# Kernel optimization log

Hardware: AMD Instinct MI355X
Metric: run time of the kernel (lower is better)

Reference implementation:

```python
import jax, jax.numpy as jnp
import numpy as np

B, N, D = 8, 1024, 512
H, HD = 8, 64          # heads, head_dim
E_EDGES = 4096         # num edges (!= N -> mean-pool branch)
NE, NSH, TOPK = 8, 2, 2  # routed experts, shared experts, top-k
DH = 2 * D             # expert hidden dim
EPS = 1e-5
HALT_BONUS = 0.1
AUX_ALPHA = 0.01


def _ln(x, g, b):
    mu = jnp.mean(x, -1, keepdims=True)
    var = jnp.mean(jnp.square(x - mu), -1, keepdims=True)
    return (x - mu) * jax.lax.rsqrt(var + EPS) * g + b


def setup_inputs() -> dict:
    key = jax.random.key(0)
    ks = jax.random.split(key, 20)
    w = lambda k, shp: jax.random.normal(k, shp, jnp.float32) * 0.02
    return {
        'h': jax.random.normal(ks[0], (B, N, D), jnp.float32),
        'edge_features': jax.random.normal(ks[1], (B, E_EDGES, D), jnp.float32),
        'log_A': jnp.zeros((D,), jnp.float32),
        'B_w': w(ks[2], (D, D)), 'B_b': jnp.zeros((D,), jnp.float32),
        'Wq': w(ks[3], (D, D)), 'bq': jnp.zeros((D,), jnp.float32),
        'Wk': w(ks[4], (D, D)), 'bk': jnp.zeros((D,), jnp.float32),
        'Wv': w(ks[5], (D, D)), 'bv': jnp.zeros((D,), jnp.float32),
        'Wo': w(ks[6], (D, D)), 'bo': jnp.zeros((D,), jnp.float32),
        'n1_g': jnp.ones((D,), jnp.float32), 'n1_b': jnp.zeros((D,), jnp.float32),
        'n2_g': jnp.ones((D,), jnp.float32), 'n2_b': jnp.zeros((D,), jnp.float32),
        'n3_g': jnp.ones((D,), jnp.float32), 'n3_b': jnp.zeros((D,), jnp.float32),
        'gate_w': w(ks[7], (D, NE)), 'gate_b': jnp.zeros((NE,), jnp.float32),
        'eW1': w(ks[8], (NE, D, DH)), 'eb1': jnp.zeros((NE, DH), jnp.float32),
        'eW2': w(ks[9], (NE, DH, D)), 'eb2': jnp.zeros((NE, D), jnp.float32),
        'sW1': w(ks[10], (NSH, D, DH)), 'sb1': jnp.zeros((NSH, DH), jnp.float32),
        'sW2': w(ks[11], (NSH, DH, D)), 'sb2': jnp.zeros((NSH, D), jnp.float32),
        'hW1': w(ks[12], (D, D // 2)), 'hb1': jnp.zeros((D // 2,), jnp.float32),
        'hW2': w(ks[13], (D // 2, 1)), 'hb2': jnp.zeros((1,), jnp.float32),
    }


def reference(h, edge_features, log_A, B_w, B_b, Wq, bq, Wk, bk, Wv, bv, Wo, bo,
              n1_g, n1_b, n2_g, n2_b, n3_g, n3_b, gate_w, gate_b,
              eW1, eb1, eW2, eb2, sW1, sb1, sW2, sb2, hW1, hb1, hW2, hb2):
    # --- LTI: h_decay + mean-pooled edge injection (num_edges != num_nodes) ---
    A = -jnp.exp(log_A)                                   # spectral constraint
    edge_inj = edge_features @ B_w + B_b                  # [B,E,D]
    edge_inj = jnp.mean(edge_inj, axis=1, keepdims=True)  # [B,1,D] broadcast
    h_lti = _ln(A * h + edge_inj, n1_g, n1_b)

    # --- attention (faithful to source: no head/node transpose -> [B,N,H,H] scores) ---
    q = (h_lti @ Wq + bq).reshape(B, N, H, HD)
    k = (h_lti @ Wk + bk).reshape(B, N, H, HD)
    v = (h_lti @ Wv + bv).reshape(B, N, H, HD)
    scores = jnp.einsum('bnhd,bngd->bnhg', q, k) / jnp.sqrt(jnp.float32(HD))
    attn = jax.nn.softmax(scores, axis=-1)                # dropout = identity (eval)
    h_attn = jnp.einsum('bnhg,bngd->bnhd', attn, v).reshape(B, N, D) @ Wo + bo
    h2 = _ln(h_lti + h_attn, n2_g, n2_b)

    # --- SparseMoE: top-k routed + shared experts, load-balance aux loss ---
    x = h2.reshape(-1, D)                                 # [T,D]
    T = x.shape[0]
    probs = jax.nn.softmax(x @ gate_w + gate_b, axis=-1)  # [T,NE]
    topv, topi = jax.lax.top_k(probs, TOPK)
    topv = topv / jnp.sum(topv, -1, keepdims=True)        # renormalize top-k
    w_full = jnp.sum(jax.nn.one_hot(topi, NE, dtype=x.dtype) * topv[..., None], axis=1)  # [T,NE]
    hid = jax.nn.silu(jnp.einsum('td,edh->teh', x, eW1) + eb1)   # [T,NE,DH]
    eout = jnp.einsum('teh,ehd->ted', hid, eW2) + eb2            # [T,NE,D]
    routed = jnp.einsum('te,ted->td', w_full, eout)
    shid = jax.nn.silu(jnp.einsum('td,sdh->tsh', x, sW1) + sb1)
    shared = jnp.sum(jnp.einsum('tsh,shd->tsd', shid, sW2) + sb2, axis=1)
    h_moe = (routed + shared).reshape(B, N, D)
    frac = jnp.mean(jnp.sum(jax.nn.one_hot(topi, NE, dtype=x.dtype), axis=1), axis=0)  # tokens per expert
    pmean = jnp.mean(probs, axis=0)
    moe_loss = AUX_ALPHA * NE * jnp.sum(frac * pmean)

    h3 = _ln(h2 + h_moe, n3_g, n3_b)                      # dropout = identity (eval)

    # --- stability loss (source uses .item() -> detached constant) ---
    stab = jax.lax.stop_gradient(jnp.maximum(jnp.max(jnp.exp(log_A)) - 0.95, 0.0))

    # --- ACT halting (cumsum_halt=None path) ---
    halt_logits = (jnp.tanh(h3 @ hW1 + hb1) @ hW2 + hb2)[..., 0]  # [B,N]
    halt_prob = jax.nn.sigmoid(halt_logits)
    cumsum_halt = halt_prob                                # zeros + prob * active(=1)
    return h3, cumsum_halt, halt_prob, stab + moe_loss
```

## Files before the change

### kernel.cpp

```cpp
#include <hip/hip_runtime.h>
#include <hip/hip_bf16.h>

#define TT 8192
#define DD 512

typedef unsigned short u16;
typedef __attribute__((ext_vector_type(8))) short short8;
typedef __attribute__((ext_vector_type(4))) float f32x4;

__device__ __forceinline__ u16 f2b(float f) {
  union { float f; unsigned int i; } w; w.f = f;
  unsigned int x = w.i;
  unsigned int r = (x + 0x7FFFu + ((x >> 16) & 1u)) >> 16;
  if ((x & 0x7F800000u) == 0x7F800000u) r = x >> 16;
  return (u16)r;
}
__device__ __forceinline__ float b2f(u16 u) {
  union { unsigned int i; float f; } w; w.i = ((unsigned int)u) << 16; return w.f;
}

__device__ __forceinline__ void blockReduce2(float& a, float& b, float* s4a, float* s4b) {
  #pragma unroll
  for (int off = 32; off; off >>= 1) { a += __shfl_xor(a, off); b += __shfl_xor(b, off); }
  int wid = threadIdx.x >> 6;
  if ((threadIdx.x & 63) == 0) { s4a[wid] = a; s4b[wid] = b; }
  __syncthreads();
  a = s4a[0] + s4a[1] + s4a[2] + s4a[3];
  b = s4b[0] + s4b[1] + s4b[2] + s4b[3];
}

__global__ __launch_bounds__(256) void k_zero(float* __restrict__ esum) {
  esum[blockIdx.x * 256 + threadIdx.x] = 0.f;
}

__global__ __launch_bounds__(256) void k_zero4(float4* __restrict__ p) {
  p[(size_t)blockIdx.x * 256 + threadIdx.x] = make_float4(0.f, 0.f, 0.f, 0.f);
}

__global__ __launch_bounds__(256) void k_esum(const float* __restrict__ ef, float* __restrict__ esum) {
  int b = blockIdx.x, ec = blockIdx.y, tid = threadIdx.x;
  float a0 = 0.f, a1 = 0.f;
  const float* base = ef + ((size_t)b * 4096 + (size_t)ec * 128) * 512;
  for (int e = 0; e < 128; ++e) {
    a0 += base[(size_t)e * 512 + tid];
    a1 += base[(size_t)e * 512 + tid + 256];
  }
  atomicAdd(&esum[b * 512 + tid], a0);
  atomicAdd(&esum[b * 512 + tid + 256], a1);
}

__global__ __launch_bounds__(256) void k_einj(const float* __restrict__ esum,
                                              const float* __restrict__ Bw, const float* __restrict__ Bb,
                                              float* __restrict__ einj) {
  int idx = blockIdx.x * 256 + threadIdx.x;
  int b = idx >> 9, dp = idx & 511;
  float a = Bb[dp];
  const float inv = 1.f / 4096.f;
  for (int d = 0; d < 512; ++d)
    a = fmaf(esum[b * 512 + d] * inv, Bw[d * 512 + dp], a);
  einj[idx] = a;
}

__global__ __launch_bounds__(256) void k_wsplit(const float* __restrict__ Wq, const float* __restrict__ Wk,
                                                const float* __restrict__ Wv, const float* __restrict__ Wo,
                                                u16* __restrict__ outh, u16* __restrict__ outl) {
  __shared__ float st[64][65];
  int z = blockIdx.z;
  const float* W = z == 0 ? Wq : (z == 1 ? Wk : (z == 2 ? Wv : Wo));
  int k0 = blockIdx.x << 6, n0 = blockIdx.y << 6;
  int tid = threadIdx.x;
  int r = tid >> 2, c4 = (tid & 3) << 4;
  #pragma unroll
  for (int j = 0; j < 16; j += 4) {
    float4 v = *(const float4*)(W + (size_t)(k0 + r) * 512 + n0 + c4 + j);
    st[c4 + j + 0][r] = v.x; st[c4 + j + 1][r] = v.y;
    st[c4 + j + 2][r] = v.z; st[c4 + j + 3][r] = v.w;
  }
  __syncthreads();
  int n = tid >> 2, kb = (tid & 3) << 4;
  u16 h8[8] __attribute__((aligned(16)));
  u16 l8[8] __attribute__((aligned(16)));
  size_t obase = (size_t)z * 262144 + (size_t)(n0 + n) * 512 + k0 + kb;
  #pragma unroll
  for (int half = 0; half < 2; ++half) {
    #pragma unroll
    for (int j = 0; j < 8; ++j) {
      float val = st[n][kb + half * 8 + j];
      h8[j] = f2b(val);
      l8[j] = f2b(val - b2f(h8[j]));
    }
    *(uint4*)(outh + obase + half * 8) = *(uint4*)h8;
    *(uint4*)(outl + obase + half * 8) = *(uint4*)l8;
  }
}

__global__ __launch_bounds__(256) void k_wt(const float* __restrict__ W, u16* __restrict__ Wt,
                                            int K, int N) {
  __shared__ float st[64][65];
  int z = blockIdx.z;
  W += (size_t)z * K * N; Wt += (size_t)z * K * N;
  int k0 = blockIdx.x << 6, n0 = blockIdx.y << 6;
  int tid = threadIdx.x;
  int r = tid >> 2, c4 = (tid & 3) << 4;
  #pragma unroll
  for (int j = 0; j < 16; j += 4) {
    float4 v = *(const float4*)(W + (size_t)(k0 + r) * N + n0 + c4 + j);
    st[c4 + j + 0][r] = v.x; st[c4 + j + 1][r] = v.y;
    st[c4 + j + 2][r] = v.z; st[c4 + j + 3][r] = v.w;
  }
  __syncthreads();
  int n = tid >> 2, kb = (tid & 3) << 4;
  u16 h8[8] __attribute__((aligned(16)));
  size_t obase = (size_t)(n0 + n) * K + k0 + kb;
  #pragma unroll
  for (int half = 0; half < 2; ++half) {
    #pragma unroll
    for (int j = 0; j < 8; ++j) h8[j] = f2b(st[n][kb + half * 8 + j]);
    *(uint4*)(Wt + obase + half * 8) = *(uint4*)h8;
  }
}

__global__ __launch_bounds__(256) void k_lti(const float* __restrict__ h, const float* __restrict__ lA,
                                             const float* __restrict__ einj,
                                             const float* __restrict__ g, const float* __restrict__ be,
                                             u16* __restrict__ Xh, u16* __restrict__ Xl, int seg0) {
  __shared__ float sa[4], sb[4];
  int rowg = seg0 + blockIdx.x, b = rowg >> 10, tid = threadIdx.x;
  int d0 = tid, d1 = tid + 256;
  size_t gbase = (size_t)rowg * 512;
  size_t lbase = (size_t)blockIdx.x * 512;
  float v0 = -expf(lA[d0]) * h[gbase + d0] + einj[b * 512 + d0];
  float v1 = -expf(lA[d1]) * h[gbase + d1] + einj[b * 512 + d1];
  float s = v0 + v1, ss = v0 * v0 + v1 * v1;
  blockReduce2(s, ss, sa, sb);
  float mu = s * (1.f / 512.f);
  float var = fmaxf(ss * (1.f / 512.f) - mu * mu, 0.f);
  float r = rsqrtf(var + 1e-5f);
  float o0 = (v0 - mu) * r * g[d0] + be[d0];
  float o1 = (v1 - mu) * r * g[d1] + be[d1];
  u16 h0 = f2b(o0), h1 = f2b(o1);
  Xh[lbase + d0] = h0; Xl[lbase + d0] = f2b(o0 - b2f(h0));
  Xh[lbase + d1] = h1; Xl[lbase + d1] = f2b(o1 - b2f(h1));
}

__global__ __launch_bounds__(256) void k_ln_res2(const u16* __restrict__ Xh, const u16* __restrict__ Xl,
                                                 const float* __restrict__ Bv,
                                                 const float* __restrict__ g, const float* __restrict__ be,
                                                 float* __restrict__ outf, u16* __restrict__ outb) {
  __shared__ float sa[4], sb[4];
  int tid = threadIdx.x, d0 = tid, d1 = tid + 256;
  size_t base = (size_t)blockIdx.x * 512;
  float v0 = b2f(Xh[base + d0]) + b2f(Xl[base + d0]) + Bv[base + d0];
  float v1 = b2f(Xh[base + d1]) + b2f(Xl[base + d1]) + Bv[base + d1];
  float s = v0 + v1, ss = v0 * v0 + v1 * v1;
  blockReduce2(s, ss, sa, sb);
  float mu = s * (1.f / 512.f);
  float var = fmaxf(ss * (1.f / 512.f) - mu * mu, 0.f);
  float r = rsqrtf(var + 1e-5f);
  float o0 = (v0 - mu) * r * g[d0] + be[d0];
  float o1 = (v1 - mu) * r * g[d1] + be[d1];
  outf[base + d0] = o0;
  outf[base + d1] = o1;
  if (outb) { outb[base + d0] = f2b(o0); outb[base + d1] = f2b(o1); }
}

__global__ __launch_bounds__(256) void k_ln_res(const float* __restrict__ A, const float* __restrict__ Bv,
                                                const float* __restrict__ g, const float* __restrict__ be,
                                                float* __restrict__ outf, u16* __restrict__ outb) {
  __shared__ float sa[4], sb[4];
  int tid = threadIdx.x, d0 = tid, d1 = tid + 256;
  size_t base = (size_t)blockIdx.x * 512;
  float v0 = A[base + d0] + Bv[base + d0];
  float v1 = A[base + d1] + Bv[base + d1];
  float s = v0 + v1, ss = v0 * v0 + v1 * v1;
  blockReduce2(s, ss, sa, sb);
  float mu = s * (1.f / 512.f);
  float var = fmaxf(ss * (1.f / 512.f) - mu * mu, 0.f);
  float r = rsqrtf(var + 1e-5f);
  float o0 = (v0 - mu) * r * g[d0] + be[d0];
  float o1 = (v1 - mu) * r * g[d1] + be[d1];
  outf[base + d0] = o0;
  outf[base + d1] = o1;
  if (outb) { outb[base + d0] = f2b(o0); outb[base + d1] = f2b(o1); }
}

template<int NOUT>
__global__ __launch_bounds__(512, 4) void gemm_sp3(
    const u16* __restrict__ Xh, const u16* __restrict__ Xl, int lda,
    const u16* __restrict__ Wth, const u16* __restrict__ Wtl,
    const float* __restrict__ b0c, const float* __restrict__ b1c, const float* __restrict__ b2c,
    float* __restrict__ C0, float* __restrict__ C1, float* __restrict__ C2) {
  const float* bias = b0c; float* C = C0;
  const u16* Wh = Wth; const u16* Wl = Wtl;
  if (NOUT == 3) {
    int z = blockIdx.z;
    Wh += (size_t)z * 262144; Wl += (size_t)z * 262144;
    if (z == 1) { bias = b1c; C = C1; }
    else if (z == 2) { bias = b2c; C = C2; }
  }
  const int bm = blockIdx.y << 7, bn = blockIdx.x << 7;
  __shared__ u16 Ah[2][128][40];
  __shared__ u16 Al[2][128][40];
  __shared__ u16 Bh[2][128][40];
  __shared__ u16 Bl[2][128][40];
  const int tid = threadIdx.x;
  const int sr = tid >> 2, sk = (tid & 3) << 3;
  const int wv = tid >> 6, lane = tid & 63, q = lane >> 4, m16 = lane & 15;
  const int wr = (wv >> 2) << 6;
  const int wc = (wv & 3) << 5;
  const u16* ahr = Xh + (size_t)(bm + sr) * lda;
  const u16* alr = Xl + (size_t)(bm + sr) * lda;
  const u16* bhr = Wh + (size_t)(bn + sr) * 512;
  const u16* blr = Wl + (size_t)(bn + sr) * 512;
  f32x4 acc[4][2];
  #pragma unroll
  for (int m = 0; m < 4; ++m)
    #pragma unroll
    for (int n = 0; n < 2; ++n)
      #pragma unroll
      for (int i = 0; i < 4; ++i) acc[m][n][i] = 0.f;

  uint4 rah = *(const uint4*)(ahr + sk);
  uint4 ral = *(const uint4*)(alr + sk);
  uint4 rbh = *(const uint4*)(bhr + sk);
  uint4 rbl = *(const uint4*)(blr + sk);
  *(uint4*)&Ah[0][sr][sk] = rah;
  *(uint4*)&Al[0][sr][sk] = ral;
  *(uint4*)&Bh[0][sr][sk] = rbh;
  *(uint4*)&Bl[0][sr][sk] = rbl;
  __syncthreads();
  int cur = 0;
  for (int k0 = 0; k0 < 512; k0 += 32) {
    if (k0 + 32 < 512) {
      rah = *(const uint4*)(ahr + k0 + 32 + sk);
      ral = *(const uint4*)(alr + k0 + 32 + sk);
      rbh = *(const uint4*)(bhr + k0 + 32 + sk);
      rbl = *(const uint4*)(blr + k0 + 32 + sk);
    }
    short8 ahf[4], alf[4];
    #pragma unroll
    for (int m = 0; m < 4; ++m) {
      ahf[m] = *(const short8*)&Ah[cur][wr + m * 16 + m16][q * 8];
      alf[m] = *(const short8*)&Al[cur][wr + m * 16 + m16][q * 8];
    }
    #pragma unroll
    for (int n = 0; n < 2; ++n) {
      short8 bhf = *(const short8*)&Bh[cur][wc + n * 16 + m16][q * 8];
      short8 blf = *(const short8*)&Bl[cur][wc + n * 16 + m16][q * 8];
      #pragma unroll
      for (int m = 0; m < 4; ++m) {
        acc[m][n] = __builtin_amdgcn_mfma_f32_16x16x32_bf16(ahf[m], bhf, acc[m][n], 0, 0, 0);
        acc[m][n] = __builtin_amdgcn_mfma_f32_16x16x32_bf16(alf[m], bhf, acc[m][n], 0, 0, 0);
        acc[m][n] = __builtin_amdgcn_mfma_f32_16x16x32_bf16(ahf[m], blf, acc[m][n], 0, 0, 0);
      }
    }
    if (k0 + 32 < 512) {
      *(uint4*)&Ah[cur ^ 1][sr][sk] = rah;
      *(uint4*)&Al[cur ^ 1][sr][sk] = ral;
      *(uint4*)&Bh[cur ^ 1][sr][sk] = rbh;
      *(uint4*)&Bl[cur ^ 1][sr][sk] = rbl;
      __syncthreads();
      cur ^= 1;
    }
  }
  #pragma unroll
  for (int n = 0; n < 2; ++n) {
    int col = bn + wc + n * 16 + m16;
    float bb = bias[col];
    #pragma unroll
    for (int m = 0; m < 4; ++m) {
      #pragma unroll
      for (int i = 0; i < 4; ++i) {
        int rl = bm + wr + m * 16 + q * 4 + i;
        C[(size_t)rl * 512 + col] = acc[m][n][i] + bb;
      }
    }
  }
}

__global__ __launch_bounds__(64) void k_attn(const float* __restrict__ q, const float* __restrict__ k,
                                             const float* __restrict__ v,
                                             u16* __restrict__ aohl) {
  __shared__ float qs[512], ks[512], vs[512], at[64];
  size_t t = blockIdx.x;
  int lane = threadIdx.x;
  for (int i = lane; i < 512; i += 64) {
    qs[i] = q[t * 512 + i]; ks[i] = k[t * 512 + i]; vs[i] = v[t * 512 + i];
  }
  __syncthreads();
  int h = lane >> 3, g = lane & 7;
  float s = 0.f;
  #pragma unroll 8
  for (int d = 0; d < 64; ++d) s = fmaf(qs[h * 64 + d], ks[g * 64 + d], s);
  s *= 0.125f;
  float m = s;
  #pragma unroll
  for (int off = 1; off < 8; off <<= 1) m = fmaxf(m, __shfl_xor(m, off));
  float ex = expf(s - m);
  float sum = ex;
  #pragma unroll
  for (int off = 1; off < 8; off <<= 1) sum += __shfl_xor(sum, off);
  at[lane] = ex / sum;
  __syncthreads();
  #pragma unroll
  for (int j = 0; j < 8; ++j) {
    int d = lane + j * 64, hh = d >> 6, hd = d & 63;
    float acc = 0.f;
    #pragma unroll
    for (int gg = 0; gg < 8; ++gg) acc = fmaf(at[hh * 8 + gg], vs[gg * 64 + hd], acc);
    u16 hi = f2b(acc);
    aohl[t * 1024 + d] = hi;
    aohl[t * 1024 + 512 + d] = f2b(acc - b2f(hi));
  }
}

__global__ __launch_bounds__(256) void k_gateA(const float* __restrict__ h2, const float* __restrict__ gw,
                                               const float* __restrict__ gb, float* __restrict__ probs,
                                               int* __restrict__ sel, float2* __restrict__ wpair) {
  int lane = threadIdx.x & 63, wid = threadIdx.x >> 6;
  int t = blockIdx.x * 4 + wid;
  const float* x = h2 + (size_t)t * 512;
  float acc[8] = {};
  for (int d = lane; d < 512; d += 64) {
    float xv = x[d];
    float4 g0 = *(const float4*)(gw + d * 8);
    float4 g1 = *(const float4*)(gw + d * 8 + 4);
    acc[0] = fmaf(xv, g0.x, acc[0]); acc[1] = fmaf(xv, g0.y, acc[1]);
    acc[2] = fmaf(xv, g0.z, acc[2]); acc[3] = fmaf(xv, g0.w, acc[3]);
    acc[4] = fmaf(xv, g1.x, acc[4]); acc[5] = fmaf(xv, g1.y, acc[5]);
    acc[6] = fmaf(xv, g1.z, acc[6]); acc[7] = fmaf(xv, g1.w, acc[7]);
  }
  #pragma unroll
  for (int off = 32; off; off >>= 1)
    #pragma unroll
    for (int e = 0; e < 8; ++e) acc[e] += __shfl_xor(acc[e], off);
  if (lane == 0) {
    float m = -1e30f;
    #pragma unroll
    for (int e = 0; e < 8; ++e) { acc[e] += gb[e]; m = fmaxf(m, acc[e]); }
    float p[8], sum = 0.f;
    #pragma unroll
    for (int e = 0; e < 8; ++e) { p[e] = expf(acc[e] - m); sum += p[e]; }
    float inv = 1.f / sum;
    #pragma unroll
    for (int e = 0; e < 8; ++e) { p[e] *= inv; probs[t * 8 + e] = p[e]; }
    int i1 = 0; float m1 = p[0];
    #pragma unroll
    for (int e = 1; e < 8; ++e) if (p[e] > m1) { m1 = p[e]; i1 = e; }
    int i2 = -1; float m2 = -1.f;
    #pragma unroll
    for (int e = 0; e < 8; ++e) if (e != i1 && p[e] > m2) { m2 = p[e]; i2 = e; }
    if (i2 < 0) i2 = (i1 + 1) & 7;
    float den = m1 + m2;
    float invs = (den > 0.f) ? 1.f / den : 0.f;
    sel[t] = i1 | (i2 << 4);
    wpair[t] = make_float2(m1 * invs, m2 * invs);
  }
}

__global__ __launch_bounds__(256) void k_gateB(const int* __restrict__ sel, const float2* __restrict__ wpair,
                                               int* __restrict__ toklist, float* __restrict__ wlist,
                                               int* __restrict__ cnt) {
  int e = blockIdx.x;
  int tid = threadIdx.x, lane = tid & 63, wv = tid >> 6;
  __shared__ int wsum[4];
  int base = 0;
  for (int t0 = 0; t0 < 8192; t0 += 256) {
    int t = t0 + tid;
    int s = sel[t];
    int i1 = s & 15, i2 = (s >> 4) & 15;
    bool f = (i1 == e) || (i2 == e);
    float wt = (i1 == e) ? wpair[t].x : ((i2 == e) ? wpair[t].y : 0.f);
    unsigned long long m = __ballot(f);
    int rank = __popcll(m & ((1ull << lane) - 1ull));
    int wtot = __popcll(m);
    if (lane == 0) wsum[wv] = wtot;
    __syncthreads();
    int prev = 0;
    for (int ww = 0; ww < wv; ++ww) prev += wsum[ww];
    int tot = wsum[0] + wsum[1] + wsum[2] + wsum[3];
    if (f) {
      int pos = base + prev + rank;
      toklist[e * 8192 + pos] = t;
      wlist[e * 8192 + pos] = wt;
    }
    base += tot;
    __syncthreads();
  }
  if (tid == 0) cnt[e] = base;
}

template<int XMODE, int ACT, int OUTMODE, int EXPERT>
__global__ __launch_bounds__(256) void mfma_gemm(
    const float* __restrict__ Xf, const u16* __restrict__ Xb,
    const float* __restrict__ Wg, const float* __restrict__ biasg,
    float* __restrict__ C, u16* __restrict__ C16,
    const int* __restrict__ toklist, const float* __restrict__ wlist,
    const int* __restrict__ cnt, int M, int K, int N, int chunk0,
    size_t hidstride, float* __restrict__ moe) {
  int e = EXPERT ? blockIdx.z : 0;
  const float* W = Wg + (size_t)e * K * N;
  const float* bias = biasg + (size_t)e * N;
  int Mloc = M;
  if (EXPERT) {
    int ce = cnt[e]; if (ce > 8192) ce = 8192;
    Mloc = ce - chunk0;
    if (XMODE == 1) Xb += (size_t)e * hidstride;
    if (OUTMODE == 2) C16 += (size_t)e * hidstride;
  }
  const int bm = blockIdx.y << 6, bn = blockIdx.x << 6;
  if (EXPERT && bm >= Mloc) return;
  __shared__ u16 As[64][40];
  __shared__ u16 Bs[64][40];
  __shared__ int rows[64];
  const int tid = threadIdx.x;
  if (EXPERT && XMODE == 2 && tid < 64) {
    int ce = cnt[e]; if (ce > 8192) ce = 8192;
    int r = chunk0 + bm + tid;
    rows[tid] = toklist[e * 8192 + (r < ce ? r : chunk0)] & 8191;
  }
  const int srow = tid >> 2;
  const int skg = (tid & 3) << 3;
  const int wv = tid >> 6, lane = tid & 63, q = lane >> 4, m16 = lane & 15;
  f32x4 acc[4];
  #pragma unroll
  for (int c = 0; c < 4; ++c)
    #pragma unroll
    for (int i = 0; i < 4; ++i) acc[c][i] = 0.f;

  for (int k0 = 0; k0 < K; k0 += 32) {
    __syncthreads();
    {
      u16 a8[8] __attribute__((aligned(16)));
      if (XMODE == 1) {
        *(uint4*)a8 = *(const uint4*)(Xb + (size_t)(bm + srow) * K + k0 + skg);
      } else {
        const float* src = (XMODE == 2) ? (Xf + (size_t)rows[srow] * K + k0 + skg)
                                        : (Xf + (size_t)(bm + srow) * K + k0 + skg);
        float4 x0 = *(const float4*)(src);
        float4 x1 = *(const float4*)(src + 4);
        a8[0] = f2b(x0.x); a8[1] = f2b(x0.y); a8[2] = f2b(x0.z); a8[3] = f2b(x0.w);
        a8[4] = f2b(x1.x); a8[5] = f2b(x1.y); a8[6] = f2b(x1.z); a8[7] = f2b(x1.w);
      }
      *(uint4*)&As[srow][skg] = *(uint4*)a8;
    }
    {
      u16 b8[8] __attribute__((aligned(16)));
      const float* src = W + (size_t)(k0 + skg) * N + bn + srow;
      #pragma unroll
      for (int j = 0; j < 8; ++j) b8[j] = f2b(src[(size_t)j * N]);
      *(uint4*)&Bs[srow][skg] = *(uint4*)b8;
    }
    __syncthreads();
    short8 af = *(const short8*)&As[wv * 16 + m16][q * 8];
    #pragma unroll
    for (int c = 0; c < 4; ++c) {
      short8 bf = *(const short8*)&Bs[c * 16 + m16][q * 8];
      acc[c] = __builtin_amdgcn_mfma_f32_16x16x32_bf16(af, bf, acc[c], 0, 0, 0);
    }
  }
  #pragma unroll
  for (int c = 0; c < 4; ++c) {
    int col = bn + c * 16 + m16;
    float bb = bias[col];
    #pragma unroll
    for (int i = 0; i < 4; ++i) {
      int rl = bm + wv * 16 + q * 4 + i;
      if (EXPERT && rl >= Mloc) continue;
      float v = acc[c][i] + bb;
      if (ACT == 1) v = v / (1.f + expf(-v));
      else if (ACT == 2) v = tanhf(v);
      if (OUTMODE == 0) C[(size_t)rl * N + col] = v;
      else if (OUTMODE == 1) C[(size_t)rl * N + col] += v;
      else if (OUTMODE == 2) C16[(size_t)rl * N + col] = f2b(v);
      else {
        int rg = chunk0 + rl;
        int tok = toklist[e * 8192 + rg] & 8191;
        float wt = wlist[e * 8192 + rg];
        atomicAdd(&moe[(size_t)tok * 512 + col], v * wt);
      }
    }
  }
}

template<int XMODE, int ACT, int OUTMODE, int EXPERT>
__global__ __launch_bounds__(512, 4) void mfma_gemm3(
    const u16* __restrict__ Xb, const u16* __restrict__ Wt, const float* __restrict__ biasg,
    float* __restrict__ C, u16* __restrict__ C16,
    const int* __restrict__ toklist, const float* __restrict__ wlist,
    const int* __restrict__ cnt, int M, int K, int N, int chunk0,
    size_t hidstride, float* __restrict__ moe) {
  int e = EXPERT ? blockIdx.z : 0;
  const u16* W = Wt + (size_t)e * K * N;
  const float* bias = biasg + (size_t)e * N;
  int Mloc = M;
  if (EXPERT == 1) {
    int ce = cnt[e]; if (ce > 8192) ce = 8192;
    Mloc = ce - chunk0;
  }
  if (EXPERT) {
    if (XMODE == 3) Xb += (size_t)e * hidstride;
    if (OUTMODE == 2) C16 += (size_t)e * hidstride;
  }
  const int bm = blockIdx.y << 7, bn = blockIdx.x << 7;
  if (EXPERT == 1 && bm >= Mloc) return;
  __shared__ u16 As[2][128][40];
  __shared__ u16 Bs[2][128][40];
  __shared__ int rows[128];
  const int tid = threadIdx.x;
  if (EXPERT == 1 && XMODE == 2) {
    if (tid < 128) {
      int ce = cnt[e]; if (ce > 8192) ce = 8192;
      int r = chunk0 + bm + tid;
      rows[tid] = toklist[e * 8192 + (r < ce ? r : chunk0)] & 8191;
    }
    __syncthreads();
  }
  const int sr = tid >> 2, sk = (tid & 3) << 3;
  const int wv = tid >> 6, lane = tid & 63, q = lane >> 4, m16 = lane & 15;
  const int wr = (wv >> 2) << 6;
  const int wc = (wv & 3) << 5;
  const u16* arow = (XMODE == 2) ? (Xb + (size_t)rows[sr] * K) : (Xb + (size_t)(bm + sr) * K);
  const u16* brow = W + (size_t)(bn + sr) * K;
  f32x4 acc[4][2];
  #pragma unroll
  for (int m = 0; m < 4; ++m)
    #pragma unroll
    for (int n = 0; n < 2; ++n)
      #pragma unroll
      for (int i = 0; i < 4; ++i) acc[m][n][i] = 0.f;

  uint4 ar = *(const uint4*)(arow + sk);
  uint4 br = *(const uint4*)(brow + sk);
  *(uint4*)&As[0][sr][sk] = ar;
  *(uint4*)&Bs[0][sr][sk] = br;
  __syncthreads();
  int cur = 0;
  for (int k0 = 0; k0 < K; k0 += 32) {
    if (k0 + 32 < K) {
      ar = *(const uint4*)(arow + k0 + 32 + sk);
      br = *(const uint4*)(brow + k0 + 32 + sk);
    }
    short8 af[4];
    #pragma unroll
    for (int m = 0; m < 4; ++m)
      af[m] = *(const short8*)&As[cur][wr + m * 16 + m16][q * 8];
    short8 bf[2];
    #pragma unroll
    for (int n = 0; n < 2; ++n)
      bf[n] = *(const short8*)&Bs[cur][wc + n * 16 + m16][q * 8];
    #pragma unroll
    for (int n = 0; n < 2; ++n)
      #pragma unroll
      for (int m = 0; m < 4; ++m)
        acc[m][n] = __builtin_amdgcn_mfma_f32_16x16x32_bf16(af[m], bf[n], acc[m][n], 0, 0, 0);
    if (k0 + 32 < K) {
      *(uint4*)&As[cur ^ 1][sr][sk] = ar;
      *(uint4*)&Bs[cur ^ 1][sr][sk] = br;
      __syncthreads();
      cur ^= 1;
    }
  }
  #pragma unroll
  for (int n = 0; n < 2; ++n) {
    int col = bn + wc + n * 16 + m16;
    float bb = bias[col];
    #pragma unroll
    for (int m = 0; m < 4; ++m) {
      #pragma unroll
      for (int i = 0; i < 4; ++i) {
        int rl = bm + wr + m * 16 + q * 4 + i;
        if (EXPERT == 1 && rl >= Mloc) continue;
        float v = acc[m][n][i] + bb;
        if (ACT == 1) v = v / (1.f + expf(-v));
        else if (ACT == 2) v = tanhf(v);
        if (OUTMODE == 0) C[(size_t)rl * N + col] = v;
        else if (OUTMODE == 1) C[(size_t)rl * N + col] += v;
        else if (OUTMODE == 2) C16[(size_t)rl * N + col] = f2b(v);
        else if (OUTMODE == 3) {
          int rg = chunk0 + rl;
          int tok = toklist[e * 8192 + rg] & 8191;
          float wt = wlist[e * 8192 + rg];
          atomicAdd(&moe[(size_t)tok * 512 + col], v * wt);
        } else {
          atomicAdd(&C[(size_t)rl * N + col], v);
        }
      }
    }
  }
}

__global__ __launch_bounds__(256) void k_halt(const u16* __restrict__ hh, const float* __restrict__ hW2,
                                              const float* __restrict__ hb2, float* __restrict__ out) {
  int lane = threadIdx.x & 63, wid = threadIdx.x >> 6;
  int t = blockIdx.x * 4 + wid;
  const u16* x = hh + (size_t)t * 256;
  float a = b2f(x[lane]) * hW2[lane] + b2f(x[lane + 64]) * hW2[lane + 64] +
            b2f(x[lane + 128]) * hW2[lane + 128] + b2f(x[lane + 192]) * hW2[lane + 192];
  #pragma unroll
  for (int off = 32; off; off >>= 1) a += __shfl_xor(a, off);
  if (lane == 0) {
    float p = 1.f / (1.f + expf(-(a + hb2[0])));
    out[4194304 + t] = p;
    out[4194304 + 8192 + t] = p;
  }
}

__global__ __launch_bounds__(256) void k_final(const float* __restrict__ probs, const int* __restrict__ cnt,
                                               const float* __restrict__ lA, float* __restrict__ out) {
  __shared__ float sp[4][8];
  __shared__ float sm[4];
  int tid = threadIdx.x, lane = tid & 63, wid = tid >> 6;
  float part[8] = {};
  for (int i = tid; i < 8192; i += 256) {
    const float* p = probs + i * 8;
    #pragma unroll
    for (int e = 0; e < 8; ++e) part[e] += p[e];
  }
  #pragma unroll
  for (int off = 32; off; off >>= 1)
    #pragma unroll
    for (int e = 0; e < 8; ++e) part[e] += __shfl_xor(part[e], off);
  float mx = 0.f;
  for (int d = tid; d < 512; d += 256) mx = fmaxf(mx, expf(lA[d]));
  #pragma unroll
  for (int off = 32; off; off >>= 1) mx = fmaxf(mx, __shfl_xor(mx, off));
  if (lane == 0) {
    #pragma unroll
    for (int e = 0; e < 8; ++e) sp[wid][e] = part[e];
    sm[wid] = mx;
  }
  __syncthreads();
  if (tid == 0) {
    float loss = 0.f;
    for (int e = 0; e < 8; ++e) {
      float pm = (sp[0][e] + sp[1][e] + sp[2][e] + sp[3][e]) * (1.f / 8192.f);
      int c = cnt[e]; if (c > 8192) c = 8192;
      loss += (float)c * (1.f / 8192.f) * pm;
    }
    loss *= 0.01f * 8.f;
    float mall = fmaxf(fmaxf(sm[0], sm[1]), fmaxf(sm[2], sm[3]));
    out[4194304 + 16384] = fmaxf(mall - 0.95f, 0.f) + loss;
  }
}

extern "C" void kernel_launch(void* const* d_in, const int* in_sizes, int n_in,
                              void* d_out, int out_size, void* d_ws, size_t ws_size,
                              hipStream_t stream) {
  const float* h   = (const float*)d_in[0];
  const float* ef  = (const float*)d_in[1];
  const float* lA  = (const float*)d_in[2];
  const float* Bw  = (const float*)d_in[3];
  const float* Bb  = (const float*)d_in[4];
  const float* Wq  = (const float*)d_in[5];  const float* bq  = (const float*)d_in[6];
  const float* Wk  = (const float*)d_in[7];  const float* bk  = (const float*)d_in[8];
  const float* Wv  = (const float*)d_in[9];  const float* bv  = (const float*)d_in[10];
  const float* Wo  = (const float*)d_in[11]; const float* bo  = (const float*)d_in[12];
  const float* n1g = (const float*)d_in[13]; const float* n1b = (const float*)d_in[14];
  const float* n2g = (const float*)d_in[15]; const float* n2b = (const float*)d_in[16];
  const float* n3g = (const float*)d_in[17]; const float* n3b = (const float*)d_in[18];
  const float* gw  = (const float*)d_in[19]; const float* gb  = (const float*)d_in[20];
  const float* eW1 = (const float*)d_in[21]; const float* eb1 = (const float*)d_in[22];
  const float* eW2 = (const float*)d_in[23]; const float* eb2 = (const float*)d_in[24];
  const float* sW1 = (const float*)d_in[25]; const float* sb1 = (const float*)d_in[26];
  const float* sW2 = (const float*)d_in[27]; const float* sb2 = (const float*)d_in[28];
  const float* hW1 = (const float*)d_in[29]; const float* hb1 = (const float*)d_in[30];
  const float* hW2 = (const float*)d_in[31]; const float* hb2 = (const float*)d_in[32];
  float* out = (float*)d_out;
  float* ws = (float*)d_ws;

  const size_t R = (size_t)TT * DD;
  const size_t SM = 155648 + 73744;
  size_t wsf = ws_size / 4;
  int S; size_t ARENA;
  bool FAST;
  if (wsf >= 6 * R + SM)      { S = 8192; ARENA = 4 * R; FAST = true; }
  else if (wsf >= 3 * R + SM) { S = 2048; ARENA = R; FAST = false; }
  else                        { S = 512;  ARENA = 1048576; FAST = false; }
  const int CAPE = (int)(ARENA / 4096);
  const int NCH  = 8192 / CAPE;
  const size_t HIDSTRIDE = (size_t)CAPE * 1024;
  const int CAPS = (ARENA / 512 >= 8192) ? 8192 : (int)(ARENA / 512);

  float* f_h2  = ws;
  float* f_moe = ws + R;
  float* arena = ws + 2 * R;
  const size_t SD = (size_t)S * 512;
  u16* f_xh = (u16*)arena;
  u16* f_xl = f_xh + SD;
  float* f_q = arena + SD;
  float* f_k = arena + 2 * SD;
  float* f_v = arena + 3 * SD;
  u16* f_aohl = (u16*)f_q;
  float* f_hp = f_k;
  u16* f_wh = (u16*)f_moe;
  u16* f_wl = f_wh + 4 * 262144;
  u16* f_hid = (u16*)arena;
  u16* f_hh  = (u16*)arena;
  u16* a16 = (u16*)arena;
  const int CAPE_F = 2048, NCH_F = 4;
  const size_t HSF = (size_t)CAPE_F * 1024;
  u16* f_hidF = a16;
  u16* f_eW1t = a16 + 16777216;
  u16* f_eW2t = a16 + 20971520;
  u16* f_h2b  = a16 + 25165824;
  u16* f_sW1t = a16 + 29360128;
  u16* f_sW2t = a16 + 30408704;
  u16* f_h3b  = a16;
  u16* f_hW1t = a16 + 4194304;
  u16* f_hh3  = a16 + 4325376;
  float* smr = ws + 2 * R + ARENA;
  float* f_esum = smr;
  float* f_einj = smr + 4096;
  float* f_probs = smr + 8192;
  float2* f_wpair = (float2*)(smr + 8192 + 65536);
  float* f_wlist = smr + 8192 + 65536 + 16384;
  int* ip = (int*)(smr + 8192 + 65536 + 16384 + 65536);
  int* sel = ip; int* cnt = ip + 8192; int* toklist = ip + 8192 + 16;

  k_zero<<<16, 256, 0, stream>>>(f_esum);
  k_esum<<<dim3(8, 32), 256, 0, stream>>>(ef, f_esum);
  k_einj<<<16, 256, 0, stream>>>(f_esum, Bw, Bb, f_einj);
  k_wsplit<<<dim3(8, 8, 4), 256, 0, stream>>>(Wq, Wk, Wv, Wo, f_wh, f_wl);

  for (int s = 0; s < TT / S; ++s) {
    int seg0 = s * S;
    k_lti<<<S, 256, 0, stream>>>(h, lA, f_einj, n1g, n1b, f_xh, f_xl, seg0);
    gemm_sp3<3><<<dim3(4, S / 128, 3), 512, 0, stream>>>(
        f_xh, f_xl, 512, f_wh, f_wl, bq, bk, bv, f_q, f_k, f_v);
    k_attn<<<S, 64, 0, stream>>>(f_q, f_k, f_v, f_aohl);
    gemm_sp3<1><<<dim3(4, S / 128, 1), 512, 0, stream>>>(
        f_aohl, f_aohl + 512, 1024, f_wh + 3 * 262144, f_wl + 3 * 262144,
        bo, nullptr, nullptr, f_hp, nullptr, nullptr);
    k_ln_res2<<<S, 256, 0, stream>>>(f_xh, f_xl, f_hp, n2g, n2b,
                                     f_h2 + (size_t)seg0 * 512,
                                     FAST ? f_h2b + (size_t)seg0 * 512 : nullptr);
  }

  k_gateA<<<TT / 4, 256, 0, stream>>>(f_h2, gw, gb, f_probs, sel, f_wpair);
  k_gateB<<<8, 256, 0, stream>>>(sel, f_wpair, toklist, f_wlist, cnt);

  if (FAST) {
    k_zero4<<<4096, 256, 0, stream>>>((float4*)f_moe);
    k_wt<<<dim3(8, 16, 8), 256, 0, stream>>>(eW1, f_eW1t, 512, 1024);
    k_wt<<<dim3(16, 8, 8), 256, 0, stream>>>(eW2, f_eW2t, 1024, 512);
    k_wt<<<dim3(8, 16, 2), 256, 0, stream>>>(sW1, f_sW1t, 512, 1024);
    k_wt<<<dim3(16, 8, 2), 256, 0, stream>>>(sW2, f_sW2t, 1024, 512);

    mfma_gemm3<1,1,2,2><<<dim3(8, 64, 2), 512, 0, stream>>>(
        f_h2b, f_sW1t, sb1, nullptr, f_hidF, nullptr, nullptr, nullptr,
        TT, 512, 1024, 0, (size_t)TT * 1024, nullptr);
    mfma_gemm3<3,0,4,2><<<dim3(4, 64, 2), 512, 0, stream>>>(
        f_hidF, f_sW2t, sb2, f_moe, nullptr, nullptr, nullptr, nullptr,
        TT, 1024, 512, 0, (size_t)TT * 1024, nullptr);

    for (int c = 0; c < NCH_F; ++c) {
      mfma_gemm3<2,1,2,1><<<dim3(8, CAPE_F / 128, 8), 512, 0, stream>>>(
          f_h2b, f_eW1t, eb1, nullptr, f_hidF, toklist, nullptr, cnt,
          CAPE_F, 512, 1024, c * CAPE_F, HSF, nullptr);
      mfma_gemm3<3,0,3,1><<<dim3(4, CAPE_F / 128, 8), 512, 0, stream>>>(
          f_hidF, f_eW2t, eb2, nullptr, nullptr, toklist, f_wlist, cnt,
          CAPE_F, 1024, 512, c * CAPE_F, HSF, f_moe);
    }

    k_ln_res<<<TT, 256, 0, stream>>>(f_h2, f_moe, n3g, n3b, out, f_h3b);
    k_wt<<<dim3(8, 4, 1), 256, 0, stream>>>(hW1, f_hW1t, 512, 256);
    mfma_gemm3<1,2,2,0><<<dim3(2, 64), 512, 0, stream>>>(
        f_h3b, f_hW1t, hb1, nullptr, f_hh3, nullptr, nullptr, nullptr,
        TT, 512, 256, 0, 0, nullptr);
    k_halt<<<TT / 4, 256, 0, stream>>>(f_hh3, hW2, hb2, out);
  } else {
    for (int sx = 0; sx < 2; ++sx)
      for (int c = 0; c < TT / CAPS; ++c) {
        const float* xs = f_h2 + (size_t)c * CAPS * 512;
        float* ms = f_moe + (size_t)c * CAPS * 512;
        mfma_gemm<0,1,2,0><<<dim3(16, CAPS / 64), 256, 0, stream>>>(
            xs, nullptr, sW1 + (size_t)sx * 524288, sb1 + sx * 1024,
            nullptr, f_hid, nullptr, nullptr, nullptr, CAPS, 512, 1024, 0, 0, nullptr);
        if (sx == 0)
          mfma_gemm<1,0,0,0><<<dim3(8, CAPS / 64), 256, 0, stream>>>(
              nullptr, f_hid, sW2, sb2, ms, nullptr, nullptr, nullptr, nullptr, CAPS, 1024, 512, 0, 0, nullptr);
        else
          mfma_gemm<1,0,1,0><<<dim3(8, CAPS / 64), 256, 0, stream>>>(
              nullptr, f_hid, sW2 + 524288, sb2 + 512, ms, nullptr, nullptr, nullptr, nullptr, CAPS, 1024, 512, 0, 0, nullptr);
      }
    for (int c = 0; c < NCH; ++c) {
      mfma_gemm<2,1,2,1><<<dim3(16, CAPE / 64, 8), 256, 0, stream>>>(
          f_h2, nullptr, eW1, eb1, nullptr, f_hid, toklist, nullptr, cnt,
          CAPE, 512, 1024, c * CAPE, HIDSTRIDE, nullptr);
      mfma_gemm<1,0,3,1><<<dim3(8, CAPE / 64, 8), 256, 0, stream>>>(
          nullptr, f_hid, eW2, eb2, nullptr, nullptr, toklist, f_wlist, cnt,
          CAPE, 1024, 512, c * CAPE, HIDSTRIDE, f_moe);
    }
    k_ln_res<<<TT, 256, 0, stream>>>(f_h2, f_moe, n3g, n3b, out, nullptr);
    mfma_gemm<0,2,2,0><<<dim3(4, 128), 256, 0, stream>>>(
        out, nullptr, hW1, hb1, nullptr, f_hh, nullptr, nullptr, nullptr, TT, 512, 256, 0, 0, nullptr);
    k_halt<<<TT / 4, 256, 0, stream>>>(f_hh, hW2, hb2, out);
  }

  k_final<<<1, 256, 0, stream>>>(f_probs, cnt, lA, out);
}
```

Before: 691.1 us.

## Pack routed experts into one grouped GEMM and fuse gating into LayerNorm

Routed-expert GEMMs now use one launch over a padded, prefix-offset packed layout: each 128-row tile looks up its expert from per-expert offsets. This replaces the four chunked launches per layer, which also spawned empty blocks for lightly loaded experts. The gate softmax and top-2 selection are fused into the second LayerNorm kernel, removing a separate pass over h2. The first shared-expert down-projection writes the output directly and the second adds into it, so the zero-fill kernel is dropped. The cost is a serial prefix-sum kernel and an 8-iteration per-block expert search. The fused gate also adds a cross-wave reduction to every LayerNorm block.

Result: faster. 637.7 us (-7.7%).

```diff
diff --git a/kernel.cpp b/kernel.cpp
--- a/kernel.cpp
+++ b/kernel.cpp
@@ -31,10 +31,6 @@
 
 __global__ __launch_bounds__(256) void k_zero(float* __restrict__ esum) {
   esum[blockIdx.x * 256 + threadIdx.x] = 0.f;
-}
-
-__global__ __launch_bounds__(256) void k_zero4(float4* __restrict__ p) {
-  p[(size_t)blockIdx.x * 256 + threadIdx.x] = make_float4(0.f, 0.f, 0.f, 0.f);
 }
 
 __global__ __launch_bounds__(256) void k_esum(const float* __restrict__ ef, float* __restrict__ esum) {
@@ -146,8 +142,12 @@
 __global__ __launch_bounds__(256) void k_ln_res2(const u16* __restrict__ Xh, const u16* __restrict__ Xl,
                                                  const float* __restrict__ Bv,
                                                  const float* __restrict__ g, const float* __restrict__ be,
-                                                 float* __restrict__ outf, u16* __restrict__ outb) {
+                                                 float* __restrict__ outf, u16* __restrict__ outb,
+                                                 const float* __restrict__ gw, const float* __restrict__ gb,
+                                                 float* __restrict__ probs, int* __restrict__ sel,
+                                                 float2* __restrict__ wpair) {
   __shared__ float sa[4], sb[4];
+  __shared__ float s8[4][8];
   int tid = threadIdx.x, d0 = tid, d1 = tid + 256;
   size_t base = (size_t)blockIdx.x * 512;
   float v0 = b2f(Xh[base + d0]) + b2f(Xl[base + d0]) + Bv[base + d0];
@@ -162,6 +162,53 @@
   outf[base + d0] = o0;
   outf[base + d1] = o1;
   if (outb) { outb[base + d0] = f2b(o0); outb[base + d1] = f2b(o1); }
+  if (probs) {
+    float4 g0a = *(const float4*)(gw + d0 * 8);
+    float4 g0b = *(const float4*)(gw + d0 * 8 + 4);
+    float4 g1a = *(const float4*)(gw + d1 * 8);
+    float4 g1b = *(const float4*)(gw + d1 * 8 + 4);
+    float ga[8] = { o0 * g0a.x + o1 * g1a.x, o0 * g0a.y + o1 * g1a.y,
+                    o0 * g0a.z + o1 * g1a.z, o0 * g0a.w + o1 * g1a.w,
+                    o0 * g0b.x + o1 * g1b.x, o0 * g0b.y + o1 * g1b.y,
+                    o0 * g0b.z + o1 * g1b.z, o0 * g0b.w + o1 * g1b.w };
+    #pragma unroll
+    for (int off = 32; off; off >>= 1)
+      #pragma unroll
+      for (int e = 0; e < 8; ++e) ga[e] += __shfl_xor(ga[e], off);
+    int lane = tid & 63, wid = tid >> 6;
+    if (lane == 0) {
+      #pragma unroll
+      for (int e = 0; e < 8; ++e) s8[wid][e] = ga[e];
+    }
+    __syncthreads();
+    if (tid == 0) {
+      int t = blockIdx.x;
+      float acc[8];
+      float m = -1e30f;
+      #pragma unroll
+      for (int e = 0; e < 8; ++e) {
+        acc[e] = s8[0][e] + s8[1][e] + s8[2][e] + s8[3][e] + gb[e];
+        m = fmaxf(m, acc[e]);
+      }
+      float p[8], sum = 0.f;
+      #pragma unroll
+      for (int e = 0; e < 8; ++e) { p[e] = expf(acc[e] - m); sum += p[e]; }
+      float inv = 1.f / sum;
+      #pragma unroll
+      for (int e = 0; e < 8; ++e) { p[e] *= inv; probs[t * 8 + e] = p[e]; }
+      int i1 = 0; float m1 = p[0];
+      #pragma unroll
+      for (int e = 1; e < 8; ++e) if (p[e] > m1) { m1 = p[e]; i1 = e; }
+      int i2 = -1; float m2 = -1.f;
+      #pragma unroll
+      for (int e = 0; e < 8; ++e) if (e != i1 && p[e] > m2) { m2 = p[e]; i2 = e; }
+      if (i2 < 0) i2 = (i1 + 1) & 7;
+      float den = m1 + m2;
+      float invs = (den > 0.f) ? 1.f / den : 0.f;
+      sel[t] = i1 | (i2 << 4);
+      wpair[t] = make_float2(m1 * invs, m2 * invs);
+    }
+  }
 }
 
 __global__ __launch_bounds__(256) void k_ln_res(const float* __restrict__ A, const float* __restrict__ Bv,
@@ -182,6 +229,17 @@
   outf[base + d0] = o0;
   outf[base + d1] = o1;
   if (outb) { outb[base + d0] = f2b(o0); outb[base + d1] = f2b(o1); }
+}
+
+__global__ __launch_bounds__(64) void k_prefix(const int* __restrict__ cnt, int* __restrict__ off) {
+  if (threadIdx.x == 0) {
+    int acc = 0;
+    for (int e = 0; e < 8; ++e) {
+      off[e] = acc;
+      int c = cnt[e]; if (c > 8192) c = 8192;
+      acc += (c + 127) & ~127;
+    }
+  }
 }
 
 template<int NOUT>
@@ -490,29 +548,46 @@
     const int* __restrict__ toklist, const float* __restrict__ wlist,
     const int* __restrict__ cnt, int M, int K, int N, int chunk0,
     size_t hidstride, float* __restrict__ moe) {
-  int e = EXPERT ? blockIdx.z : 0;
+  const int bm = blockIdx.y << 7, bn = blockIdx.x << 7;
+  int e = 0, offe = 0;
+  int Mloc = M;
+  if (EXPERT == 1) {
+    e = blockIdx.z;
+    int ce = cnt[e]; if (ce > 8192) ce = 8192;
+    Mloc = ce - chunk0;
+    if (bm >= Mloc) return;
+  } else if (EXPERT == 2) {
+    e = blockIdx.z;
+  } else if (EXPERT == 3) {
+    const int* off = cnt + 8;
+    int found = -1;
+    #pragma unroll
+    for (int ee = 0; ee < 8; ++ee) {
+      int c = cnt[ee]; if (c > 8192) c = 8192;
+      int st = off[ee], len = (c + 127) & ~127;
+      if (found < 0 && bm >= st && bm < st + len) found = ee;
+    }
+    if (found < 0) return;
+    e = found; offe = off[e];
+    int ce = cnt[e]; if (ce > 8192) ce = 8192;
+    Mloc = offe + ce;
+    if (bm >= Mloc) return;
+  }
   const u16* W = Wt + (size_t)e * K * N;
   const float* bias = biasg + (size_t)e * N;
-  int Mloc = M;
-  if (EXPERT == 1) {
-    int ce = cnt[e]; if (ce > 8192) ce = 8192;
-    Mloc = ce - chunk0;
-  }
-  if (EXPERT) {
+  if (EXPERT == 1 || EXPERT == 2) {
     if (XMODE == 3) Xb += (size_t)e * hidstride;
     if (OUTMODE == 2) C16 += (size_t)e * hidstride;
   }
-  const int bm = blockIdx.y << 7, bn = blockIdx.x << 7;
-  if (EXPERT == 1 && bm >= Mloc) return;
   __shared__ u16 As[2][128][40];
   __shared__ u16 Bs[2][128][40];
   __shared__ int rows[128];
   const int tid = threadIdx.x;
-  if (EXPERT == 1 && XMODE == 2) {
+  if (XMODE == 2) {
     if (tid < 128) {
       int ce = cnt[e]; if (ce > 8192) ce = 8192;
-      int r = chunk0 + bm + tid;
-      rows[tid] = toklist[e * 8192 + (r < ce ? r : chunk0)] & 8191;
+      int r = (EXPERT == 3) ? (bm - offe + tid) : (chunk0 + bm + tid);
+      rows[tid] = toklist[e * 8192 + (r < ce ? r : (ce > 0 ? ce - 1 : 0))] & 8191;
     }
     __syncthreads();
   }
@@ -570,7 +645,7 @@
       #pragma unroll
       for (int i = 0; i < 4; ++i) {
         int rl = bm + wr + m * 16 + q * 4 + i;
-        if (EXPERT == 1 && rl >= Mloc) continue;
+        if ((EXPERT == 1 || EXPERT == 3) && rl >= Mloc) continue;
         float v = acc[m][n][i] + bb;
         if (ACT == 1) v = v / (1.f + expf(-v));
         else if (ACT == 2) v = tanhf(v);
@@ -578,7 +653,7 @@
         else if (OUTMODE == 1) C[(size_t)rl * N + col] += v;
         else if (OUTMODE == 2) C16[(size_t)rl * N + col] = f2b(v);
         else if (OUTMODE == 3) {
-          int rg = chunk0 + rl;
+          int rg = (EXPERT == 3) ? (rl - offe) : (chunk0 + rl);
           int tok = toklist[e * 8192 + rg] & 8191;
           float wt = wlist[e * 8192 + rg];
           atomicAdd(&moe[(size_t)tok * 512 + col], v * wt);
@@ -698,14 +773,12 @@
   u16* f_hid = (u16*)arena;
   u16* f_hh  = (u16*)arena;
   u16* a16 = (u16*)arena;
-  const int CAPE_F = 2048, NCH_F = 4;
-  const size_t HSF = (size_t)CAPE_F * 1024;
-  u16* f_hidF = a16;
-  u16* f_eW1t = a16 + 16777216;
-  u16* f_eW2t = a16 + 20971520;
-  u16* f_h2b  = a16 + 25165824;
-  u16* f_sW1t = a16 + 29360128;
-  u16* f_sW2t = a16 + 30408704;
+  u16* f_hidC = a16;
+  u16* f_eW1t = a16 + 17825792;
+  u16* f_eW2t = a16 + 22020096;
+  u16* f_h2b  = a16 + 26214400;
+  u16* f_sW1t = a16 + 30408704;
+  u16* f_sW2t = a16 + 31457280;
   u16* f_h3b  = a16;
   u16* f_hW1t = a16 + 4194304;
   u16* f_hh3  = a16 + 4325376;
@@ -716,7 +789,7 @@
   float2* f_wpair = (float2*)(smr + 8192 + 65536);
   float* f_wlist = smr + 8192 + 65536 + 16384;
   int* ip = (int*)(smr + 8192 + 65536 + 16384 + 65536);
-  int* sel = ip; int* cnt = ip + 8192; int* toklist = ip + 8192 + 16;
+  int* sel = ip; int* cnt = ip + 8192; int* off = ip + 8192 + 8; int* toklist = ip + 8192 + 16;
 
   k_zero<<<16, 256, 0, stream>>>(f_esum);
   k_esum<<<dim3(8, 32), 256, 0, stream>>>(ef, f_esum);
@@ -732,36 +805,42 @@
     gemm_sp3<1><<<dim3(4, S / 128, 1), 512, 0, stream>>>(
         f_aohl, f_aohl + 512, 1024, f_wh + 3 * 262144, f_wl + 3 * 262144,
         bo, nullptr, nullptr, f_hp, nullptr, nullptr);
-    k_ln_res2<<<S, 256, 0, stream>>>(f_xh, f_xl, f_hp, n2g, n2b,
-                                     f_h2 + (size_t)seg0 * 512,
-                                     FAST ? f_h2b + (size_t)seg0 * 512 : nullptr);
-  }
-
-  k_gateA<<<TT / 4, 256, 0, stream>>>(f_h2, gw, gb, f_probs, sel, f_wpair);
+    if (FAST)
+      k_ln_res2<<<S, 256, 0, stream>>>(f_xh, f_xl, f_hp, n2g, n2b,
+                                       f_h2, f_h2b, gw, gb, f_probs, sel, f_wpair);
+    else
+      k_ln_res2<<<S, 256, 0, stream>>>(f_xh, f_xl, f_hp, n2g, n2b,
+                                       f_h2 + (size_t)seg0 * 512, nullptr,
+                                       nullptr, nullptr, nullptr, nullptr, nullptr);
+  }
+
+  if (!FAST)
+    k_gateA<<<TT / 4, 256, 0, stream>>>(f_h2, gw, gb, f_probs, sel, f_wpair);
   k_gateB<<<8, 256, 0, stream>>>(sel, f_wpair, toklist, f_wlist, cnt);
 
   if (FAST) {
-    k_zero4<<<4096, 256, 0, stream>>>((float4*)f_moe);
+    k_prefix<<<1, 64, 0, stream>>>(cnt, off);
     k_wt<<<dim3(8, 16, 8), 256, 0, stream>>>(eW1, f_eW1t, 512, 1024);
     k_wt<<<dim3(16, 8, 8), 256, 0, stream>>>(eW2, f_eW2t, 1024, 512);
     k_wt<<<dim3(8, 16, 2), 256, 0, stream>>>(sW1, f_sW1t, 512, 1024);
     k_wt<<<dim3(16, 8, 2), 256, 0, stream>>>(sW2, f_sW2t, 1024, 512);
 
     mfma_gemm3<1,1,2,2><<<dim3(8, 64, 2), 512, 0, stream>>>(
-        f_h2b, f_sW1t, sb1, nullptr, f_hidF, nullptr, nullptr, nullptr,
+        f_h2b, f_sW1t, sb1, nullptr, f_hidC, nullptr, nullptr, nullptr,
         TT, 512, 1024, 0, (size_t)TT * 1024, nullptr);
-    mfma_gemm3<3,0,4,2><<<dim3(4, 64, 2), 512, 0, stream>>>(
-        f_hidF, f_sW2t, sb2, f_moe, nullptr, nullptr, nullptr, nullptr,
-        TT, 1024, 512, 0, (size_t)TT * 1024, nullptr);
-
-    for (int c = 0; c < NCH_F; ++c) {
-      mfma_gemm3<2,1,2,1><<<dim3(8, CAPE_F / 128, 8), 512, 0, stream>>>(
-          f_h2b, f_eW1t, eb1, nullptr, f_hidF, toklist, nullptr, cnt,
-          CAPE_F, 512, 1024, c * CAPE_F, HSF, nullptr);
-      mfma_gemm3<3,0,3,1><<<dim3(4, CAPE_F / 128, 8), 512, 0, stream>>>(
-          f_hidF, f_eW2t, eb2, nullptr, nullptr, toklist, f_wlist, cnt,
-          CAPE_F, 1024, 512, c * CAPE_F, HSF, f_moe);
-    }
+    mfma_gemm3<1,0,0,0><<<dim3(4, 64), 512, 0, stream>>>(
+        f_hidC, f_sW2t, sb2, f_moe, nullptr, nullptr, nullptr, nullptr,
+        TT, 1024, 512, 0, 0, nullptr);
+    mfma_gemm3<1,0,1,0><<<dim3(4, 64), 512, 0, stream>>>(
+        f_hidC + (size_t)TT * 1024, f_sW2t + 524288, sb2 + 512, f_moe, nullptr,
+        nullptr, nullptr, nullptr, TT, 1024, 512, 0, 0, nullptr);
+
+    mfma_gemm3<2,1,2,3><<<dim3(8, 136), 512, 0, stream>>>(
+        f_h2b, f_eW1t, eb1, nullptr, f_hidC, toklist, nullptr, cnt,
+        0, 512, 1024, 0, 0, nullptr);
+    mfma_gemm3<1,0,3,3><<<dim3(4, 136), 512, 0, stream>>>(
+        f_hidC, f_eW2t, eb2, nullptr, nullptr, toklist, f_wlist, cnt,
+        0, 1024, 512, 0, 0, f_moe);
 
     k_ln_res<<<TT, 256, 0, stream>>>(f_h2, f_moe, n3g, n3b, out, f_h3b);
     k_wt<<<dim3(8, 4, 1), 256, 0, stream>>>(hW1, f_hW1t, 512, 256);
```
